# Optimization experiments

Measured on AMD Instinct MI355X. Metric: run time of the kernel, lower is better.

## Reference

```python
import jax, jax.numpy as jnp
import numpy as np

N = 100_000      # num nodes
E = 1_600_000    # num edges
DIN, H, L, NQ = 3, 64, 5, 50_000
BN_EPS = 1e-5


def setup_inputs() -> dict:
    key = jax.random.key(0)
    ks = jax.random.split(key, 24)
    f = lambda k, s, sc=1.0: jax.random.normal(k, s, dtype=jnp.float32) * sc
    inv = 1.0 / np.sqrt(H)
    return {
        "x": f(ks[0], (N, DIN)),
        "edge_index": jax.random.randint(ks[1], (2, E), 0, N, dtype=jnp.int32),
        "n_qubits": NQ,
        "w_in": f(ks[2], (DIN, H), 0.5),
        "b_in": f(ks[3], (H,), 0.1),
        "msg_w1": f(ks[4], (L, H, H), inv),
        "msg_b1": f(ks[5], (L, H), 0.1),
        "msg_w2": f(ks[6], (L, H, H), inv),
        "msg_b2": f(ks[7], (L, H), 0.1),
        "upd_w1": f(ks[8], (L, 2 * H, H), 1.0 / np.sqrt(2 * H)),
        "upd_b1": f(ks[9], (L, H), 0.1),
        "upd_w2": f(ks[10], (L, H, H), inv),
        "upd_b2": f(ks[11], (L, H), 0.1),
        "bn_g": jax.random.uniform(ks[12], (L, H), jnp.float32, 0.5, 1.5),
        "bn_b": f(ks[13], (L, H), 0.1),
        "bn_m": f(ks[14], (L, H), 0.1),
        "bn_v": jax.random.uniform(ks[15], (L, H), jnp.float32, 0.5, 1.5),
        "out_w1": f(ks[16], (H, H // 2), inv),
        "out_b1": f(ks[17], (H // 2,), 0.1),
        "out_w2": f(ks[18], (H // 2, 1), 1.0 / np.sqrt(H // 2)),
        "out_b2": f(ks[19], (1,), 0.1),
    }


def reference(x, edge_index, n_qubits, w_in, b_in,
              msg_w1, msg_b1, msg_w2, msg_b2,
              upd_w1, upd_b1, upd_w2, upd_b2,
              bn_g, bn_b, bn_m, bn_v,
              out_w1, out_b1, out_w2, out_b2):
    src, dst = edge_index[0], edge_index[1]  # PyG: x_j = x[src], aggregate at dst
    h = jax.nn.relu(x @ w_in + b_in)         # [N, H]
    for i in range(L):
        xj = h[src]                                                    # gather [E, H]
        m = jax.nn.relu(xj @ msg_w1[i] + msg_b1[i]) @ msg_w2[i] + msg_b2[i]
        agg = jax.ops.segment_sum(m, dst, num_segments=N)              # scatter-add [N, H]
        comb = jnp.concatenate([h, agg], axis=-1)                      # [N, 2H]
        hn = jax.nn.relu(comb @ upd_w1[i] + upd_b1[i]) @ upd_w2[i] + upd_b2[i]
        # BatchNorm1d (eval mode: running stats) + residual + relu (dropout=eval identity)
        hn = (hn - bn_m[i]) * jax.lax.rsqrt(bn_v[i] + BN_EPS) * bn_g[i] + bn_b[i]
        h = jax.nn.relu(hn + h)
    q = h[:n_qubits]                                                   # qubit nodes [NQ, H]
    return jax.nn.relu(q @ out_w1 + out_b1) @ out_w2 + out_b2          # [NQ, 1]
```

## Files before the change

kernel.cpp:

```cpp
#include <hip/hip_runtime.h>
#include <hip/hip_bf16.h>

#define H 64
#define PADW 88
#define PADT 68
#define CAP 10240
#define WSTRIDE 20480

typedef __attribute__((ext_vector_type(8))) short short8;
typedef __attribute__((ext_vector_type(4))) short short4v;
typedef __attribute__((ext_vector_type(4))) float floatx4;

#define MFMA(a, b, c) __builtin_amdgcn_mfma_f32_16x16x32_bf16(a, b, c, 0, 0, 0)

__device__ __forceinline__ float bf2f(short s) {
  union { unsigned int u; float f; } v;
  v.u = ((unsigned int)(unsigned short)s) << 16;
  return v.f;
}
__device__ __forceinline__ short f2bf(float f) {
  union { float f; unsigned int u; } v; v.f = f;
  unsigned int r = v.u + 0x7fffu + ((v.u >> 16) & 1u);
  return (short)(r >> 16);
}
__device__ __forceinline__ void split2(float v, short& hi, short& lo) {
  hi = f2bf(v);
  lo = f2bf(v - bf2f(hi));
}
__device__ __forceinline__ unsigned int cvtpk(float a, float b) {
  unsigned int r;
  asm("v_cvt_pk_bf16_f32 %0, %1, %2" : "=v"(r) : "v"(a), "v"(b));
  return r;
}
__device__ __forceinline__ short f2bf1(float f) { return (short)cvtpk(f, f); }
__device__ __forceinline__ void split2a(float v, short& hi, short& lo) {
  unsigned int h = cvtpk(v, v);
  union { unsigned int u; float f; } t; t.u = h << 16;
  hi = (short)h;
  float res = v - t.f;
  lo = (short)cvtpk(res, res);
}
__device__ __forceinline__ void split16pk(const float* av, short8* thi, short8* tlo) {
  union U8 { short8 s; unsigned int u[4]; } H0, L0, H1, L1;
#pragma unroll
  for (int p = 0; p < 4; ++p) {
    float v0 = av[2 * p], v1 = av[2 * p + 1];
    unsigned int h = cvtpk(v0, v1);
    union { unsigned int u; float f; } a, b;
    a.u = h << 16; b.u = h & 0xffff0000u;
    H0.u[p] = h; L0.u[p] = cvtpk(v0 - a.f, v1 - b.f);
    float w0 = av[8 + 2 * p], w1 = av[8 + 2 * p + 1];
    unsigned int g = cvtpk(w0, w1);
    union { unsigned int u; float f; } c, d;
    c.u = g << 16; d.u = g & 0xffff0000u;
    H1.u[p] = g; L1.u[p] = cvtpk(w0 - c.f, w1 - d.f);
  }
  thi[0] = H0.s; tlo[0] = L0.s; thi[1] = H1.s; tlo[1] = L1.s;
}
__device__ __forceinline__ float ldf(const void* p, long idx, bool isf32) {
  return isf32 ? ((const float*)p)[idx] : bf2f(((const short*)p)[idx]);
}

__global__ void k_probe(const short* __restrict__ x, int* __restrict__ flag) {
  __shared__ int cnt;
  if (threadIdx.x == 0) cnt = 0;
  __syncthreads();
  short s = x[threadIdx.x];
  int e = (s >> 7) & 0xFF;
  int insane = (e != 0 && (e < 100 || e > 140)) ? 1 : 0;
  atomicAdd(&cnt, insane);
  __syncthreads();
  if (threadIdx.x == 0) *flag = (cnt > 64) ? 1 : 0;
}

__global__ void k_input2(const void* __restrict__ x, const void* __restrict__ w,
                         const void* __restrict__ b, short* __restrict__ hhi,
                         short* __restrict__ hlo, const int* __restrict__ flag, int N) {
  bool isf32 = (*flag != 0);
  int idx = blockIdx.x * 256 + threadIdx.x;
  if (idx >= N * H) return;
  int v = idx >> 6, k = idx & 63;
  float acc = ldf(b, k, isf32);
#pragma unroll
  for (int d = 0; d < 3; ++d)
    acc += ldf(x, (long)v * 3 + d, isf32) * ldf(w, d * 64 + k, isf32);
  float r = fmaxf(acc, 0.f);
  short hi, lo; split2a(r, hi, lo);
  hhi[idx] = hi; hlo[idx] = lo;
}

__global__ void k_prep(const void* __restrict__ U1, const void* __restrict__ U2,
                       const void* __restrict__ W1m, const void* __restrict__ W2m,
                       short* __restrict__ prep, const int* __restrict__ flag) {
  bool isf32 = (*flag != 0);
  int i = blockIdx.x;
  short* p = prep + (long)i * WSTRIDE;
  long oU = (long)i * 8192, oW = (long)i * 4096;
  for (int idx = threadIdx.x; idx < 8192; idx += 256) {
    int in = idx >> 6, n = idx & 63;
    int t = n >> 4, mm = n & 15, c = in >> 5, qq = (in >> 3) & 3, jj = in & 7;
    p[(((t * 4 + c) * 64) + (qq * 16 + mm)) * 8 + jj] = f2bf(ldf(U1, oU + idx, isf32));
  }
  for (int idx = threadIdx.x; idx < 4096; idx += 256) {
    int in = idx >> 6, n = idx & 63;
    int t = n >> 4, mm = n & 15, c = in >> 5, qq = (in >> 3) & 3, jj = in & 7;
    int fi = (((t * 2 + c) * 64) + (qq * 16 + mm)) * 8 + jj;
    p[8192 + fi]  = f2bf(ldf(U2, oW + idx, isf32));
    p[12288 + fi] = f2bf(ldf(W1m, oW + idx, isf32));
    p[16384 + fi] = f2bf(ldf(W2m, oW + idx, isf32));
  }
}


__global__ void k_bcount(const int* __restrict__ dstI, int* __restrict__ bcnt, int E) {
  __shared__ int cl[1024];
  int tid = threadIdx.x;
  for (int t = tid; t < 1024; t += 256) cl[t] = 0;
  __syncthreads();
  for (int i = blockIdx.x * 256 + tid; i < E; i += gridDim.x * 256)
    atomicAdd(&cl[dstI[i] >> 8], 1);
  __syncthreads();
  for (int t = tid; t < 1024; t += 256)
    if (cl[t]) atomicAdd(&bcnt[t], cl[t]);
}

__global__ void k_bscan(const int* __restrict__ bcnt, int* __restrict__ bbase,
                        int* __restrict__ bcur) {
  __shared__ int s[256];
  int tid = threadIdx.x;
  int base = tid * 4;
  int v0 = bcnt[base], v1 = bcnt[base + 1], v2 = bcnt[base + 2], v3 = bcnt[base + 3];
  int tsum = v0 + v1 + v2 + v3;
  s[tid] = tsum;
  __syncthreads();
  for (int off = 1; off < 256; off <<= 1) {
    int x = (tid >= off) ? s[tid - off] : 0;
    __syncthreads();
    s[tid] += x;
    __syncthreads();
  }
  int excl = s[tid] - tsum;
  bbase[base] = excl;           bcur[base] = excl;
  bbase[base + 1] = excl + v0;  bcur[base + 1] = excl + v0;
  bbase[base + 2] = excl + v0 + v1;      bcur[base + 2] = excl + v0 + v1;
  bbase[base + 3] = excl + v0 + v1 + v2; bcur[base + 3] = excl + v0 + v1 + v2;
  if (tid == 255) bbase[1024] = s[255];
}

__global__ void k_bin(const int* __restrict__ srcI, const int* __restrict__ dstI,
                      int* __restrict__ bcur, int2* __restrict__ pairs, int E) {
  __shared__ int cl[1024], cur[1024];
  int tid = threadIdx.x;
  int chunk = (E + gridDim.x - 1) / gridDim.x;
  int s = blockIdx.x * chunk;
  int e = min(s + chunk, E);
  for (int t = tid; t < 1024; t += 256) cl[t] = 0;
  __syncthreads();
  for (int i = s + tid; i < e; i += 256) atomicAdd(&cl[dstI[i] >> 8], 1);
  __syncthreads();
  for (int t = tid; t < 1024; t += 256)
    cur[t] = cl[t] ? atomicAdd(&bcur[t], cl[t]) : 0;
  __syncthreads();
  for (int i = s + tid; i < e; i += 256) {
    int d = dstI[i];
    int p = atomicAdd(&cur[d >> 8], 1);
    pairs[p] = (int2){srcI[i], d};
  }
}

__global__ __launch_bounds__(256) void k_sortb(
    const int2* __restrict__ pairs, const int* __restrict__ bbase,
    int* __restrict__ rowptr, int* __restrict__ srcS, int N, int E, int B) {
  __shared__ int cnt[256], cur[256], s2[256];
  __shared__ int stage[CAP];
  int b = blockIdx.x, tid = threadIdx.x;
  int lo = b << 8;
  int W = min(256, N - lo);
  int s = bbase[b], e = bbase[b + 1];
  cnt[tid] = 0;
  __syncthreads();
  for (int i = s + tid; i < e; i += 256)
    atomicAdd(&cnt[pairs[i].y - lo], 1);
  __syncthreads();
  int v = (tid < W) ? cnt[tid] : 0;
  s2[tid] = v;
  __syncthreads();
  for (int off = 1; off < 256; off <<= 1) {
    int x = (tid >= off) ? s2[tid - off] : 0;
    __syncthreads();
    s2[tid] += x;
    __syncthreads();
  }
  int excl = s2[tid] - v;
  if (tid < W) {
    rowptr[lo + tid] = s + excl;
    cur[tid] = excl;
  }
  if (b == B - 1 && tid == 0) rowptr[N] = E;
  __syncthreads();
  for (int i = s + tid; i < e; i += 256) {
    int2 pr = pairs[i];
    int p = atomicAdd(&cur[pr.y - lo], 1);
    if (p < CAP) stage[p] = pr.x;
    else srcS[s + p] = pr.x;
  }
  __syncthreads();
  int Sb = e - s;
  int lim = Sb < CAP ? Sb : CAP;
  for (int i = tid; i < lim; i += 256) srcS[s + i] = stage[i];
}

__global__ __launch_bounds__(256) void k_mlp(
    const short* __restrict__ hhi, const short* __restrict__ hlo,
    const void* __restrict__ W1, const void* __restrict__ B1,
    const void* __restrict__ W2, long oW, long oB,
    short* __restrict__ M, const int* __restrict__ flag, int N) {
  __shared__ short w1hi[64 * PADW], w1lo[64 * PADW];
  __shared__ short w2hi[64 * PADW], w2lo[64 * PADW];
  __shared__ float b1s[64];
  __shared__ float tbuf[4][16 * PADT];

  bool isf32 = (*flag != 0);
  int tid = threadIdx.x;
  for (int idx = tid; idx < 4096; idx += 256) {
    int j = idx >> 6, k = idx & 63;
    short hi, lo;
    split2a(ldf(W1, oW + idx, isf32), hi, lo);
    w1hi[k * PADW + j] = hi; w1lo[k * PADW + j] = lo;
    split2a(ldf(W2, oW + idx, isf32), hi, lo);
    w2hi[k * PADW + j] = hi; w2lo[k * PADW + j] = lo;
  }
  if (tid < 64) b1s[tid] = ldf(B1, oB + tid, isf32);
  __syncthreads();

  const int wave = tid >> 6, lane = tid & 63;
  const int m = lane & 15, quad = lane >> 4;
  float* tb = tbuf[wave];

  for (int nb = blockIdx.x * 64; nb < N; nb += gridDim.x * 64) {
    const int nBase = nb + wave * 16;
    int node = nBase + m;
    int nc = node < N ? node : N - 1;

    short8 fhi[2], flo[2];
    fhi[0] = *(const short8*)(hhi + (long)nc * H + quad * 8);
    fhi[1] = *(const short8*)(hhi + (long)nc * H + 32 + quad * 8);
    flo[0] = *(const short8*)(hlo + (long)nc * H + quad * 8);
    flo[1] = *(const short8*)(hlo + (long)nc * H + 32 + quad * 8);

    floatx4 acc[4];
#pragma unroll
    for (int t = 0; t < 4; ++t) acc[t] = (floatx4){0.f, 0.f, 0.f, 0.f};
#pragma unroll
    for (int t = 0; t < 4; ++t) {
      const short* whi = &w1hi[(t * 16 + m) * PADW + quad * 8];
      const short* wlo = &w1lo[(t * 16 + m) * PADW + quad * 8];
      acc[t] = MFMA(fhi[0], *(const short8*)(whi), acc[t]);
      acc[t] = MFMA(fhi[1], *(const short8*)(whi + 32), acc[t]);
      acc[t] = MFMA(flo[0], *(const short8*)(whi), acc[t]);
      acc[t] = MFMA(flo[1], *(const short8*)(whi + 32), acc[t]);
      acc[t] = MFMA(fhi[0], *(const short8*)(wlo), acc[t]);
      acc[t] = MFMA(fhi[1], *(const short8*)(wlo + 32), acc[t]);
    }

#pragma unroll
    for (int t = 0; t < 4; ++t) {
      int col = t * 16 + m;
      float bb = b1s[col];
#pragma unroll
      for (int r = 0; r < 4; ++r)
        tb[(quad * 4 + r) * PADT + col] = fmaxf(acc[t][r] + bb, 0.f);
    }

    float av[16];
    *(floatx4*)(av + 0)  = *(const floatx4*)(&tb[m * PADT + quad * 8]);
    *(floatx4*)(av + 4)  = *(const floatx4*)(&tb[m * PADT + quad * 8 + 4]);
    *(floatx4*)(av + 8)  = *(const floatx4*)(&tb[m * PADT + 32 + quad * 8]);
    *(floatx4*)(av + 12) = *(const floatx4*)(&tb[m * PADT + 32 + quad * 8 + 4]);
    short8 thi[2], tlo[2];
    split16pk(av, thi, tlo);

    floatx4 mac[4];
#pragma unroll
    for (int t = 0; t < 4; ++t) mac[t] = (floatx4){0.f, 0.f, 0.f, 0.f};
#pragma unroll
    for (int t = 0; t < 4; ++t) {
      const short* whi = &w2hi[(t * 16 + m) * PADW + quad * 8];
      const short* wlo = &w2lo[(t * 16 + m) * PADW + quad * 8];
      mac[t] = MFMA(thi[0], *(const short8*)(whi), mac[t]);
      mac[t] = MFMA(thi[1], *(const short8*)(whi + 32), mac[t]);
      mac[t] = MFMA(tlo[0], *(const short8*)(whi), mac[t]);
      mac[t] = MFMA(tlo[1], *(const short8*)(whi + 32), mac[t]);
      mac[t] = MFMA(thi[0], *(const short8*)(wlo), mac[t]);
      mac[t] = MFMA(thi[1], *(const short8*)(wlo + 32), mac[t]);
    }

#pragma unroll
    for (int t = 0; t < 4; ++t) {
      int col = t * 16 + m;
#pragma unroll
      for (int r = 0; r < 4; ++r) {
        int nrow = nBase + quad * 4 + r;
        if (nrow < N) M[(long)nrow * H + col] = f2bf1(mac[t][r]);
      }
    }
  }
}

__global__ __launch_bounds__(256) void k_gather(
    const short* __restrict__ M, const int* __restrict__ rowptr,
    const int* __restrict__ srcS, const void* __restrict__ B2, long oB,
    short* __restrict__ agg, const int* __restrict__ flag, int N, int totWaves) {
  __shared__ float b2s[64];
  bool isf32 = (*flag != 0);
  if (threadIdx.x < 64) b2s[threadIdx.x] = ldf(B2, oB + threadIdx.x, isf32);
  __syncthreads();
  const int wave = threadIdx.x >> 6, lane = threadIdx.x & 63;
  const int g = lane >> 3, l = lane & 7;
  float b2v[8];
#pragma unroll
  for (int j = 0; j < 8; ++j) b2v[j] = b2s[l * 8 + j];

  const int gw = blockIdx.x * 4 + wave;
  const int nTask = (N + 7) >> 3;
  for (int task = gw; task < nTask; task += totWaves) {
    int n = task * 8 + g;
    bool valid = n < N;
    int nc = valid ? n : N - 1;
    int rs = rowptr[nc], re = rowptr[nc + 1];
    if (!valid) { rs = 0; re = 0; }
    float a[8];
#pragma unroll
    for (int j = 0; j < 8; ++j) a[j] = 0.f;
    int fullEnd = rs + ((re - rs) & ~7);
    int e = rs;
    for (; e < fullEnd; e += 8) {
      int sv[8];
#pragma unroll
      for (int u = 0; u < 8; ++u) sv[u] = srcS[e + u];
      short8 rr[8];
#pragma unroll
      for (int u = 0; u < 8; ++u)
        rr[u] = *(const short8*)(M + (long)sv[u] * H + l * 8);
#pragma unroll
      for (int u = 0; u < 8; ++u) {
#pragma unroll
        for (int j = 0; j < 8; ++j) a[j] += bf2f(rr[u][j]);
      }
    }
    if (e < re) {
      short8 rr[8];
#pragma unroll
      for (int u = 0; u < 8; ++u) {
        if (e + u < re)
          rr[u] = *(const short8*)(M + (long)srcS[e + u] * H + l * 8);
      }
#pragma unroll
      for (int u = 0; u < 8; ++u) {
        if (e + u < re) {
#pragma unroll
          for (int j = 0; j < 8; ++j) a[j] += bf2f(rr[u][j]);
        }
      }
    }
    if (valid) {
      float dv = (float)(re - rs);
      union { short8 s; unsigned int u[4]; } o;
#pragma unroll
      for (int p = 0; p < 4; ++p)
        o.u[p] = cvtpk(a[2 * p] + dv * b2v[2 * p], a[2 * p + 1] + dv * b2v[2 * p + 1]);
      *(short8*)(agg + (long)n * H + l * 8) = o.s;
    }
  }
}

__global__ __launch_bounds__(512, 4) void k_updm(
    short* __restrict__ hhi, short* __restrict__ hlo, const short* __restrict__ agg,
    const short* __restrict__ pw, const short* __restrict__ pwn,
    const void* __restrict__ UB1, const void* __restrict__ UB2,
    const void* __restrict__ G, const void* __restrict__ Bb,
    const void* __restrict__ Mm, const void* __restrict__ Vv,
    const void* __restrict__ B1m,
    long oB, long oBn,
    short* __restrict__ Mout, const int* __restrict__ flag, int N, int doMsg) {
  __shared__ short u1f[8192];
  __shared__ short u2f[4096];
  __shared__ short m1f[4096];
  __shared__ float b1s[64], b2s[64], scl[64], sft[64], mb1[64];
  __shared__ float tbuf[8][16 * PADT];

  bool isf32 = (*flag != 0);
  int tid = threadIdx.x;
  const int wave = tid >> 6, lane = tid & 63;
  const int m = lane & 15, quad = lane >> 4;

  for (int c = tid; c < 1024; c += 512)
    ((short8*)u1f)[c] = ((const short8*)pw)[c];
  for (int c = tid; c < 512; c += 512) {
    ((short8*)u2f)[c] = ((const short8*)(pw + 8192))[c];
    ((short8*)m1f)[c] = ((const short8*)(pwn + 12288))[c];
  }
  short8 m2r[4][2];
#pragma unroll
  for (int t = 0; t < 4; ++t)
#pragma unroll
    for (int c = 0; c < 2; ++c)
      m2r[t][c] = *(const short8*)&pwn[16384 + (((t * 2 + c) * 64) + lane) * 8];
  if (tid < 64) {
    b1s[tid] = ldf(UB1, oB + tid, isf32);
    b2s[tid] = ldf(UB2, oB + tid, isf32);
    float s = ldf(G, oB + tid, isf32) * rsqrtf(ldf(Vv, oB + tid, isf32) + 1e-5f);
    scl[tid] = s;
    sft[tid] = ldf(Bb, oB + tid, isf32) - ldf(Mm, oB + tid, isf32) * s;
    mb1[tid] = ldf(B1m, oBn + tid, isf32);
  }
  __syncthreads();

  float* tb = tbuf[wave];

  for (int nb = blockIdx.x * 128; nb < N; nb += gridDim.x * 128) {
    const int nBase = nb + wave * 16;
    int node = nBase + m;
    int nc = node < N ? node : N - 1;

    short8 fhi[4], flo[2];
    fhi[0] = *(const short8*)(hhi + (long)nc * H + quad * 8);
    fhi[1] = *(const short8*)(hhi + (long)nc * H + 32 + quad * 8);
    flo[0] = *(const short8*)(hlo + (long)nc * H + quad * 8);
    flo[1] = *(const short8*)(hlo + (long)nc * H + 32 + quad * 8);
    fhi[2] = *(const short8*)(agg + (long)nc * H + quad * 8);
    fhi[3] = *(const short8*)(agg + (long)nc * H + 32 + quad * 8);

    floatx4 acc[4];
#pragma unroll
    for (int t = 0; t < 4; ++t) acc[t] = (floatx4){0.f, 0.f, 0.f, 0.f};
#pragma unroll
    for (int t = 0; t < 4; ++t) {
#pragma unroll
      for (int c = 0; c < 4; ++c) {
        const short8 w = *(const short8*)&u1f[(((t * 4 + c) * 64) + lane) * 8];
        acc[t] = MFMA(fhi[c], w, acc[t]);
        if (c < 2) acc[t] = MFMA(flo[c], w, acc[t]);
      }
    }

#pragma unroll
    for (int t = 0; t < 4; ++t) {
      int col = t * 16 + m;
      float bb = b1s[col];
#pragma unroll
      for (int r = 0; r < 4; ++r)
        tb[(quad * 4 + r) * PADT + col] = fmaxf(acc[t][r] + bb, 0.f);
    }
    float av[16];
    *(floatx4*)(av + 0)  = *(const floatx4*)(&tb[m * PADT + quad * 8]);
    *(floatx4*)(av + 4)  = *(const floatx4*)(&tb[m * PADT + quad * 8 + 4]);
    *(floatx4*)(av + 8)  = *(const floatx4*)(&tb[m * PADT + 32 + quad * 8]);
    *(floatx4*)(av + 12) = *(const floatx4*)(&tb[m * PADT + 32 + quad * 8 + 4]);
    short8 thi[2], tlo[2];
    split16pk(av, thi, tlo);

    floatx4 mac[4];
#pragma unroll
    for (int t = 0; t < 4; ++t) mac[t] = (floatx4){0.f, 0.f, 0.f, 0.f};
#pragma unroll
    for (int t = 0; t < 4; ++t) {
#pragma unroll
      for (int c = 0; c < 2; ++c) {
        const short8 w = *(const short8*)&u2f[(((t * 2 + c) * 64) + lane) * 8];
        mac[t] = MFMA(thi[c], w, mac[t]);
        mac[t] = MFMA(tlo[c], w, mac[t]);
      }
    }

#pragma unroll
    for (int t = 0; t < 4; ++t) {
      int col = t * 16 + m;
      float bb = b2s[col], ss = scl[col], ff = sft[col];
#pragma unroll
      for (int r = 0; r < 4; ++r)
        tb[(quad * 4 + r) * PADT + col] = (mac[t][r] + bb) * ss + ff;
    }
    *(floatx4*)(av + 0)  = *(const floatx4*)(&tb[m * PADT + quad * 8]);
    *(floatx4*)(av + 4)  = *(const floatx4*)(&tb[m * PADT + quad * 8 + 4]);
    *(floatx4*)(av + 8)  = *(const floatx4*)(&tb[m * PADT + 32 + quad * 8]);
    *(floatx4*)(av + 12) = *(const floatx4*)(&tb[m * PADT + 32 + quad * 8 + 4]);
    float hn[16];
#pragma unroll
    for (int j = 0; j < 8; ++j) {
      hn[j]     = fmaxf(av[j]     + bf2f(fhi[0][j]) + bf2f(flo[0][j]), 0.f);
      hn[8 + j] = fmaxf(av[8 + j] + bf2f(fhi[1][j]) + bf2f(flo[1][j]), 0.f);
    }
    split16pk(hn, thi, tlo);
    if (node < N) {
      long base = (long)node * H;
      *(short8*)(hhi + base + quad * 8)      = thi[0];
      *(short8*)(hhi + base + 32 + quad * 8) = thi[1];
      *(short8*)(hlo + base + quad * 8)      = tlo[0];
      *(short8*)(hlo + base + 32 + quad * 8) = tlo[1];
    }

    if (doMsg) {
#pragma unroll
      for (int t = 0; t < 4; ++t) acc[t] = (floatx4){0.f, 0.f, 0.f, 0.f};
#pragma unroll
      for (int t = 0; t < 4; ++t) {
#pragma unroll
        for (int c = 0; c < 2; ++c) {
          const short8 w = *(const short8*)&m1f[(((t * 2 + c) * 64) + lane) * 8];
          acc[t] = MFMA(thi[c], w, acc[t]);
          acc[t] = MFMA(tlo[c], w, acc[t]);
        }
      }

#pragma unroll
      for (int t = 0; t < 4; ++t) {
        int col = t * 16 + m;
        float bb = mb1[col];
#pragma unroll
        for (int r = 0; r < 4; ++r)
          tb[(quad * 4 + r) * PADT + col] = fmaxf(acc[t][r] + bb, 0.f);
      }
      *(floatx4*)(av + 0)  = *(const floatx4*)(&tb[m * PADT + quad * 8]);
      *(floatx4*)(av + 4)  = *(const floatx4*)(&tb[m * PADT + quad * 8 + 4]);
      *(floatx4*)(av + 8)  = *(const floatx4*)(&tb[m * PADT + 32 + quad * 8]);
      *(floatx4*)(av + 12) = *(const floatx4*)(&tb[m * PADT + 32 + quad * 8 + 4]);
      split16pk(av, thi, tlo);

#pragma unroll
      for (int t = 0; t < 4; ++t) mac[t] = (floatx4){0.f, 0.f, 0.f, 0.f};
#pragma unroll
      for (int t = 0; t < 4; ++t) {
#pragma unroll
        for (int c = 0; c < 2; ++c) {
          mac[t] = MFMA(thi[c], m2r[t][c], mac[t]);
          mac[t] = MFMA(tlo[c], m2r[t][c], mac[t]);
        }
      }

#pragma unroll
      for (int t = 0; t < 4; ++t) {
        int col = t * 16 + m;
#pragma unroll
        for (int r = 0; r < 4; ++r)
          tb[(quad * 4 + r) * PADT + col] = mac[t][r];
      }
      *(floatx4*)(av + 0)  = *(const floatx4*)(&tb[m * PADT + quad * 8]);
      *(floatx4*)(av + 4)  = *(const floatx4*)(&tb[m * PADT + quad * 8 + 4]);
      *(floatx4*)(av + 8)  = *(const floatx4*)(&tb[m * PADT + 32 + quad * 8]);
      *(floatx4*)(av + 12) = *(const floatx4*)(&tb[m * PADT + 32 + quad * 8 + 4]);
      if (node < N) {
        union { short8 s; unsigned int u[4]; } M0, M1;
#pragma unroll
        for (int p = 0; p < 4; ++p) {
          M0.u[p] = cvtpk(av[2 * p], av[2 * p + 1]);
          M1.u[p] = cvtpk(av[8 + 2 * p], av[8 + 2 * p + 1]);
        }
        long base = (long)node * H;
        *(short8*)(Mout + base + quad * 8)      = M0.s;
        *(short8*)(Mout + base + 32 + quad * 8) = M1.s;
      }
    }
  }
}

__global__ __launch_bounds__(256) void k_out2(
    const short* __restrict__ hhi, const short* __restrict__ hlo,
    const void* __restrict__ W1, const void* __restrict__ B1,
    const void* __restrict__ W2, const void* __restrict__ B2,
    void* __restrict__ out, const int* __restrict__ flag, int NQ) {
  __shared__ float w1s[64 * 32];
  __shared__ float b1sh[32], w2s[32];
  bool isf32 = (*flag != 0);
  int tid = threadIdx.x;
  for (int idx = tid; idx < 2048; idx += 256) w1s[idx] = ldf(W1, idx, isf32);
  if (tid < 32) { b1sh[tid] = ldf(B1, tid, isf32); w2s[tid] = ldf(W2, tid, isf32); }
  __syncthreads();
  int v = blockIdx.x * 256 + tid;
  if (v >= NQ) return;
  float hr[64];
#pragma unroll
  for (int j = 0; j < 64; ++j)
    hr[j] = bf2f(hhi[(long)v * H + j]) + bf2f(hlo[(long)v * H + j]);
  float accum = ldf(B2, 0, isf32);
#pragma unroll 4
  for (int k = 0; k < 32; ++k) {
    float t = b1sh[k];
#pragma unroll
    for (int j = 0; j < 64; ++j) t += hr[j] * w1s[j * 32 + k];
    accum += fmaxf(t, 0.f) * w2s[k];
  }
  if (isf32) ((float*)out)[v] = accum;
  else ((short*)out)[v] = f2bf1(accum);
}

extern "C" void kernel_launch(void* const* d_in, const int* in_sizes, int n_in,
                              void* d_out, int out_size, void* d_ws, size_t ws_size,
                              hipStream_t stream) {
  const void* x      = d_in[0];
  const int*  ei     = (const int*)d_in[1];
  const void* w_in   = d_in[3];
  const void* b_in   = d_in[4];
  const void* msg_w1 = d_in[5];
  const void* msg_b1 = d_in[6];
  const void* msg_w2 = d_in[7];
  const void* msg_b2 = d_in[8];
  const void* upd_w1 = d_in[9];
  const void* upd_b1 = d_in[10];
  const void* upd_w2 = d_in[11];
  const void* upd_b2 = d_in[12];
  const void* bn_g   = d_in[13];
  const void* bn_b   = d_in[14];
  const void* bn_m   = d_in[15];
  const void* bn_v   = d_in[16];
  const void* out_w1 = d_in[17];
  const void* out_b1 = d_in[18];
  const void* out_w2 = d_in[19];
  const void* out_b2 = d_in[20];

  const int N = in_sizes[0] / 3;
  const int E = in_sizes[1] / 2;
  const int L = in_sizes[5] / (H * H);
  const int* srcI = ei;
  const int* dstI = ei + E;
  const int B = (N + 255) >> 8;

  size_t off = 0;
  auto alloc = [&](size_t bytes) { size_t o = off; off += (bytes + 255) & ~(size_t)255; return o; };
  size_t mSize = (size_t)N * H * sizeof(short);
  size_t pSize = (size_t)E * sizeof(int2);
  size_t o_flag   = alloc(256);
  size_t o_bcnt   = alloc(1024 * sizeof(int));
  size_t o_bbase  = alloc(1025 * sizeof(int));
  size_t o_bcur   = alloc(1024 * sizeof(int));
  size_t o_prep   = alloc((size_t)L * WSTRIDE * sizeof(short));
  size_t o_hhi    = alloc((size_t)N * H * sizeof(short));
  size_t o_hlo    = alloc((size_t)N * H * sizeof(short));
  size_t o_agg    = alloc((size_t)N * H * sizeof(short));
  size_t o_M      = alloc(mSize > pSize ? mSize : pSize);
  size_t o_rowptr = alloc((size_t)(N + 1) * sizeof(int));
  size_t o_srcS   = alloc((size_t)E * sizeof(int));

  char* ws = (char*)d_ws;
  int*   flag   = (int*)(ws + o_flag);
  int*   bcnt   = (int*)(ws + o_bcnt);
  int*   bbase  = (int*)(ws + o_bbase);
  int*   bcur   = (int*)(ws + o_bcur);
  short* prep   = (short*)(ws + o_prep);
  short* hhi    = (short*)(ws + o_hhi);
  short* hlo    = (short*)(ws + o_hlo);
  short* aggS   = (short*)(ws + o_agg);
  short* Mbuf   = (short*)(ws + o_M);
  int2*  pairs  = (int2*)(ws + o_M);
  int*   rowptr = (int*)(ws + o_rowptr);
  int*   srcS   = (int*)(ws + o_srcS);

  k_probe<<<1, 256, 0, stream>>>((const short*)x, flag);
  k_prep<<<L, 256, 0, stream>>>(upd_w1, upd_w2, msg_w1, msg_w2, prep, flag);
  k_input2<<<(N * H + 255) / 256, 256, 0, stream>>>(x, w_in, b_in, hhi, hlo, flag, N);

  hipMemsetAsync(bcnt, 0, 1024 * sizeof(int), stream);
  k_bcount<<<256, 256, 0, stream>>>(dstI, bcnt, E);
  k_bscan<<<1, 256, 0, stream>>>(bcnt, bbase, bcur);
  k_bin<<<256, 256, 0, stream>>>(srcI, dstI, bcur, pairs, E);
  k_sortb<<<B, 256, 0, stream>>>(pairs, bbase, rowptr, srcS, N, E, B);

  k_mlp<<<768, 256, 0, stream>>>(hhi, hlo,
      msg_w1, msg_b1, msg_w2, 0, 0, Mbuf, flag, N);

  const int nTask = (N + 7) >> 3;
  const int GB = (nTask + 7) / 8;
  const int UB = (N + 255) / 256;
  for (int i = 0; i < L; ++i) {
    long oB = (long)i * H;
    int doMsg = (i + 1 < L) ? 1 : 0;
    int iN = doMsg ? i + 1 : i;
    long oBn = doMsg ? (long)(i + 1) * H : 0;
    k_gather<<<GB, 256, 0, stream>>>(Mbuf, rowptr, srcS,
        msg_b2, oB, aggS, flag, N, GB * 4);
    k_updm<<<UB, 512, 0, stream>>>(hhi, hlo, aggS,
        prep + (size_t)i * WSTRIDE, prep + (size_t)iN * WSTRIDE,
        upd_b1, upd_b2, bn_g, bn_b, bn_m, bn_v, msg_b1,
        oB, oBn, Mbuf, flag, N, doMsg);
  }
  k_out2<<<(out_size + 255) / 256, 256, 0, stream>>>(hhi, hlo,
      out_w1, out_b1, out_w2, out_b2, d_out, flag, out_size);
}
```

Measured before the change: 508.8 us.

## Fuse per-layer gather and update kernels into one persistent cooperative kernel

Replaces the per-layer pair of k_gather and k_updm launches with a single cooperative kernel, k_layers, that loops over all layers. Each layer runs a gather phase and an update/message phase, separated by grid-wide barriers. Per-layer weights are reloaded into shared memory inside the loop. This removes repeated kernel launches and the gaps between them, at the cost of grid.sync overhead. It also caps the grid at a size set by occupancy, so the gather phase may run with fewer resident waves than the standalone kernel had.

```diff
diff --git a/kernel.cpp b/kernel.cpp
--- a/kernel.cpp
+++ b/kernel.cpp
@@ -1,5 +1,8 @@
 #include <hip/hip_runtime.h>
 #include <hip/hip_bf16.h>
+#include <hip/hip_cooperative_groups.h>
+
+namespace cg = cooperative_groups;
 
 #define H 64
 #define PADW 88
@@ -22,10 +25,6 @@
   union { float f; unsigned int u; } v; v.f = f;
   unsigned int r = v.u + 0x7fffu + ((v.u >> 16) & 1u);
   return (short)(r >> 16);
-}
-__device__ __forceinline__ void split2(float v, short& hi, short& lo) {
-  hi = f2bf(v);
-  lo = f2bf(v - bf2f(hi));
 }
 __device__ __forceinline__ unsigned int cvtpk(float a, float b) {
   unsigned int r;
@@ -307,82 +306,18 @@
   }
 }
 
-__global__ __launch_bounds__(256) void k_gather(
-    const short* __restrict__ M, const int* __restrict__ rowptr,
-    const int* __restrict__ srcS, const void* __restrict__ B2, long oB,
-    short* __restrict__ agg, const int* __restrict__ flag, int N, int totWaves) {
-  __shared__ float b2s[64];
-  bool isf32 = (*flag != 0);
-  if (threadIdx.x < 64) b2s[threadIdx.x] = ldf(B2, oB + threadIdx.x, isf32);
-  __syncthreads();
-  const int wave = threadIdx.x >> 6, lane = threadIdx.x & 63;
-  const int g = lane >> 3, l = lane & 7;
-  float b2v[8];
-#pragma unroll
-  for (int j = 0; j < 8; ++j) b2v[j] = b2s[l * 8 + j];
-
-  const int gw = blockIdx.x * 4 + wave;
-  const int nTask = (N + 7) >> 3;
-  for (int task = gw; task < nTask; task += totWaves) {
-    int n = task * 8 + g;
-    bool valid = n < N;
-    int nc = valid ? n : N - 1;
-    int rs = rowptr[nc], re = rowptr[nc + 1];
-    if (!valid) { rs = 0; re = 0; }
-    float a[8];
-#pragma unroll
-    for (int j = 0; j < 8; ++j) a[j] = 0.f;
-    int fullEnd = rs + ((re - rs) & ~7);
-    int e = rs;
-    for (; e < fullEnd; e += 8) {
-      int sv[8];
-#pragma unroll
-      for (int u = 0; u < 8; ++u) sv[u] = srcS[e + u];
-      short8 rr[8];
-#pragma unroll
-      for (int u = 0; u < 8; ++u)
-        rr[u] = *(const short8*)(M + (long)sv[u] * H + l * 8);
-#pragma unroll
-      for (int u = 0; u < 8; ++u) {
-#pragma unroll
-        for (int j = 0; j < 8; ++j) a[j] += bf2f(rr[u][j]);
-      }
-    }
-    if (e < re) {
-      short8 rr[8];
-#pragma unroll
-      for (int u = 0; u < 8; ++u) {
-        if (e + u < re)
-          rr[u] = *(const short8*)(M + (long)srcS[e + u] * H + l * 8);
-      }
-#pragma unroll
-      for (int u = 0; u < 8; ++u) {
-        if (e + u < re) {
-#pragma unroll
-          for (int j = 0; j < 8; ++j) a[j] += bf2f(rr[u][j]);
-        }
-      }
-    }
-    if (valid) {
-      float dv = (float)(re - rs);
-      union { short8 s; unsigned int u[4]; } o;
-#pragma unroll
-      for (int p = 0; p < 4; ++p)
-        o.u[p] = cvtpk(a[2 * p] + dv * b2v[2 * p], a[2 * p + 1] + dv * b2v[2 * p + 1]);
-      *(short8*)(agg + (long)n * H + l * 8) = o.s;
-    }
-  }
-}
-
-__global__ __launch_bounds__(512, 4) void k_updm(
-    short* __restrict__ hhi, short* __restrict__ hlo, const short* __restrict__ agg,
-    const short* __restrict__ pw, const short* __restrict__ pwn,
+__global__ __launch_bounds__(512, 4) void k_layers(
+    short* __restrict__ hhi, short* __restrict__ hlo,
+    short* __restrict__ aggS, short* __restrict__ Mbuf,
+    const short* __restrict__ prep, const int* __restrict__ rowptr,
+    const int* __restrict__ srcS,
     const void* __restrict__ UB1, const void* __restrict__ UB2,
     const void* __restrict__ G, const void* __restrict__ Bb,
     const void* __restrict__ Mm, const void* __restrict__ Vv,
-    const void* __restrict__ B1m,
-    long oB, long oBn,
-    short* __restrict__ Mout, const int* __restrict__ flag, int N, int doMsg) {
+    const void* __restrict__ B1m, const void* __restrict__ B2m,
+    const int* __restrict__ flag, int N, int L) {
+  cg::grid_group grid = cg::this_grid();
+
   __shared__ short u1f[8192];
   __shared__ short u2f[4096];
   __shared__ short m1f[4096];
@@ -393,174 +328,244 @@
   int tid = threadIdx.x;
   const int wave = tid >> 6, lane = tid & 63;
   const int m = lane & 15, quad = lane >> 4;
-
-  for (int c = tid; c < 1024; c += 512)
-    ((short8*)u1f)[c] = ((const short8*)pw)[c];
-  for (int c = tid; c < 512; c += 512) {
-    ((short8*)u2f)[c] = ((const short8*)(pw + 8192))[c];
-    ((short8*)m1f)[c] = ((const short8*)(pwn + 12288))[c];
-  }
-  short8 m2r[4][2];
-#pragma unroll
-  for (int t = 0; t < 4; ++t)
-#pragma unroll
-    for (int c = 0; c < 2; ++c)
-      m2r[t][c] = *(const short8*)&pwn[16384 + (((t * 2 + c) * 64) + lane) * 8];
-  if (tid < 64) {
-    b1s[tid] = ldf(UB1, oB + tid, isf32);
-    b2s[tid] = ldf(UB2, oB + tid, isf32);
-    float s = ldf(G, oB + tid, isf32) * rsqrtf(ldf(Vv, oB + tid, isf32) + 1e-5f);
-    scl[tid] = s;
-    sft[tid] = ldf(Bb, oB + tid, isf32) - ldf(Mm, oB + tid, isf32) * s;
-    mb1[tid] = ldf(B1m, oBn + tid, isf32);
-  }
-  __syncthreads();
-
   float* tb = tbuf[wave];
 
-  for (int nb = blockIdx.x * 128; nb < N; nb += gridDim.x * 128) {
-    const int nBase = nb + wave * 16;
-    int node = nBase + m;
-    int nc = node < N ? node : N - 1;
-
-    short8 fhi[4], flo[2];
-    fhi[0] = *(const short8*)(hhi + (long)nc * H + quad * 8);
-    fhi[1] = *(const short8*)(hhi + (long)nc * H + 32 + quad * 8);
-    flo[0] = *(const short8*)(hlo + (long)nc * H + quad * 8);
-    flo[1] = *(const short8*)(hlo + (long)nc * H + 32 + quad * 8);
-    fhi[2] = *(const short8*)(agg + (long)nc * H + quad * 8);
-    fhi[3] = *(const short8*)(agg + (long)nc * H + 32 + quad * 8);
-
-    floatx4 acc[4];
-#pragma unroll
-    for (int t = 0; t < 4; ++t) acc[t] = (floatx4){0.f, 0.f, 0.f, 0.f};
-#pragma unroll
-    for (int t = 0; t < 4; ++t) {
-#pragma unroll
-      for (int c = 0; c < 4; ++c) {
-        const short8 w = *(const short8*)&u1f[(((t * 4 + c) * 64) + lane) * 8];
-        acc[t] = MFMA(fhi[c], w, acc[t]);
-        if (c < 2) acc[t] = MFMA(flo[c], w, acc[t]);
-      }
-    }
-
-#pragma unroll
-    for (int t = 0; t < 4; ++t) {
-      int col = t * 16 + m;
-      float bb = b1s[col];
-#pragma unroll
-      for (int r = 0; r < 4; ++r)
-        tb[(quad * 4 + r) * PADT + col] = fmaxf(acc[t][r] + bb, 0.f);
-    }
-    float av[16];
-    *(floatx4*)(av + 0)  = *(const floatx4*)(&tb[m * PADT + quad * 8]);
-    *(floatx4*)(av + 4)  = *(const floatx4*)(&tb[m * PADT + quad * 8 + 4]);
-    *(floatx4*)(av + 8)  = *(const floatx4*)(&tb[m * PADT + 32 + quad * 8]);
-    *(floatx4*)(av + 12) = *(const floatx4*)(&tb[m * PADT + 32 + quad * 8 + 4]);
-    short8 thi[2], tlo[2];
-    split16pk(av, thi, tlo);
-
-    floatx4 mac[4];
-#pragma unroll
-    for (int t = 0; t < 4; ++t) mac[t] = (floatx4){0.f, 0.f, 0.f, 0.f};
-#pragma unroll
-    for (int t = 0; t < 4; ++t) {
-#pragma unroll
-      for (int c = 0; c < 2; ++c) {
-        const short8 w = *(const short8*)&u2f[(((t * 2 + c) * 64) + lane) * 8];
-        mac[t] = MFMA(thi[c], w, mac[t]);
-        mac[t] = MFMA(tlo[c], w, mac[t]);
-      }
-    }
-
-#pragma unroll
-    for (int t = 0; t < 4; ++t) {
-      int col = t * 16 + m;
-      float bb = b2s[col], ss = scl[col], ff = sft[col];
-#pragma unroll
-      for (int r = 0; r < 4; ++r)
-        tb[(quad * 4 + r) * PADT + col] = (mac[t][r] + bb) * ss + ff;
-    }
-    *(floatx4*)(av + 0)  = *(const floatx4*)(&tb[m * PADT + quad * 8]);
-    *(floatx4*)(av + 4)  = *(const floatx4*)(&tb[m * PADT + quad * 8 + 4]);
-    *(floatx4*)(av + 8)  = *(const floatx4*)(&tb[m * PADT + 32 + quad * 8]);
-    *(floatx4*)(av + 12) = *(const floatx4*)(&tb[m * PADT + 32 + quad * 8 + 4]);
-    float hn[16];
-#pragma unroll
-    for (int j = 0; j < 8; ++j) {
-      hn[j]     = fmaxf(av[j]     + bf2f(fhi[0][j]) + bf2f(flo[0][j]), 0.f);
-      hn[8 + j] = fmaxf(av[8 + j] + bf2f(fhi[1][j]) + bf2f(flo[1][j]), 0.f);
-    }
-    split16pk(hn, thi, tlo);
-    if (node < N) {
-      long base = (long)node * H;
-      *(short8*)(hhi + base + quad * 8)      = thi[0];
-      *(short8*)(hhi + base + 32 + quad * 8) = thi[1];
-      *(short8*)(hlo + base + quad * 8)      = tlo[0];
-      *(short8*)(hlo + base + 32 + quad * 8) = tlo[1];
-    }
-
-    if (doMsg) {
+  for (int i = 0; i < L; ++i) {
+    long oB = (long)i * H;
+    int doMsg = (i + 1 < L) ? 1 : 0;
+    int iN = doMsg ? i + 1 : i;
+    long oBn = doMsg ? (long)(i + 1) * H : 0;
+    const short* pw  = prep + (size_t)i * WSTRIDE;
+    const short* pwn = prep + (size_t)iN * WSTRIDE;
+
+    for (int c = tid; c < 1024; c += 512)
+      ((short8*)u1f)[c] = ((const short8*)pw)[c];
+    for (int c = tid; c < 512; c += 512) {
+      ((short8*)u2f)[c] = ((const short8*)(pw + 8192))[c];
+      ((short8*)m1f)[c] = ((const short8*)(pwn + 12288))[c];
+    }
+    short8 m2r[4][2];
+#pragma unroll
+    for (int t = 0; t < 4; ++t)
+#pragma unroll
+      for (int c = 0; c < 2; ++c)
+        m2r[t][c] = *(const short8*)&pwn[16384 + (((t * 2 + c) * 64) + lane) * 8];
+    if (tid < 64) {
+      b1s[tid] = ldf(UB1, oB + tid, isf32);
+      b2s[tid] = ldf(UB2, oB + tid, isf32);
+      float s = ldf(G, oB + tid, isf32) * rsqrtf(ldf(Vv, oB + tid, isf32) + 1e-5f);
+      scl[tid] = s;
+      sft[tid] = ldf(Bb, oB + tid, isf32) - ldf(Mm, oB + tid, isf32) * s;
+      mb1[tid] = ldf(B1m, oBn + tid, isf32);
+    }
+
+    {
+      const int g = lane >> 3, l = lane & 7;
+      float b2v[8];
+#pragma unroll
+      for (int j = 0; j < 8; ++j) b2v[j] = ldf(B2m, oB + l * 8 + j, isf32);
+      const int totW = gridDim.x * 8;
+      const int gw = blockIdx.x * 8 + wave;
+      const int nTask = (N + 7) >> 3;
+      for (int task = gw; task < nTask; task += totW) {
+        int n = task * 8 + g;
+        bool valid = n < N;
+        int nc2 = valid ? n : N - 1;
+        int rs = rowptr[nc2], re = rowptr[nc2 + 1];
+        if (!valid) { rs = 0; re = 0; }
+        float a[8];
+#pragma unroll
+        for (int j = 0; j < 8; ++j) a[j] = 0.f;
+        int fullEnd = rs + ((re - rs) & ~7);
+        int e = rs;
+        for (; e < fullEnd; e += 8) {
+          int sv[8];
+#pragma unroll
+          for (int u = 0; u < 8; ++u) sv[u] = srcS[e + u];
+          short8 rr[8];
+#pragma unroll
+          for (int u = 0; u < 8; ++u)
+            rr[u] = *(const short8*)(Mbuf + (long)sv[u] * H + l * 8);
+#pragma unroll
+          for (int u = 0; u < 8; ++u) {
+#pragma unroll
+            for (int j = 0; j < 8; ++j) a[j] += bf2f(rr[u][j]);
+          }
+        }
+        if (e < re) {
+          short8 rr[8];
+#pragma unroll
+          for (int u = 0; u < 8; ++u) {
+            if (e + u < re)
+              rr[u] = *(const short8*)(Mbuf + (long)srcS[e + u] * H + l * 8);
+          }
+#pragma unroll
+          for (int u = 0; u < 8; ++u) {
+            if (e + u < re) {
+#pragma unroll
+              for (int j = 0; j < 8; ++j) a[j] += bf2f(rr[u][j]);
+            }
+          }
+        }
+        if (valid) {
+          float dv = (float)(re - rs);
+          union { short8 s; unsigned int u[4]; } o;
+#pragma unroll
+          for (int p = 0; p < 4; ++p)
+            o.u[p] = cvtpk(a[2 * p] + dv * b2v[2 * p], a[2 * p + 1] + dv * b2v[2 * p + 1]);
+          *(short8*)(aggS + (long)n * H + l * 8) = o.s;
+        }
+      }
+    }
+
+    grid.sync();
+
+    for (int nb = blockIdx.x * 128; nb < N; nb += gridDim.x * 128) {
+      const int nBase = nb + wave * 16;
+      int node = nBase + m;
+      int nc = node < N ? node : N - 1;
+
+      short8 fhi[4], flo[2];
+      fhi[0] = *(const short8*)(hhi + (long)nc * H + quad * 8);
+      fhi[1] = *(const short8*)(hhi + (long)nc * H + 32 + quad * 8);
+      flo[0] = *(const short8*)(hlo + (long)nc * H + quad * 8);
+      flo[1] = *(const short8*)(hlo + (long)nc * H + 32 + quad * 8);
+      fhi[2] = *(const short8*)(aggS + (long)nc * H + quad * 8);
+      fhi[3] = *(const short8*)(aggS + (long)nc * H + 32 + quad * 8);
+
+      floatx4 acc[4];
 #pragma unroll
       for (int t = 0; t < 4; ++t) acc[t] = (floatx4){0.f, 0.f, 0.f, 0.f};
 #pragma unroll
       for (int t = 0; t < 4; ++t) {
 #pragma unroll
-        for (int c = 0; c < 2; ++c) {
-          const short8 w = *(const short8*)&m1f[(((t * 2 + c) * 64) + lane) * 8];
-          acc[t] = MFMA(thi[c], w, acc[t]);
-          acc[t] = MFMA(tlo[c], w, acc[t]);
+        for (int c = 0; c < 4; ++c) {
+          const short8 w = *(const short8*)&u1f[(((t * 4 + c) * 64) + lane) * 8];
+          acc[t] = MFMA(fhi[c], w, acc[t]);
+          if (c < 2) acc[t] = MFMA(flo[c], w, acc[t]);
         }
       }
 
 #pragma unroll
       for (int t = 0; t < 4; ++t) {
         int col = t * 16 + m;
-        float bb = mb1[col];
+        float bb = b1s[col];
 #pragma unroll
         for (int r = 0; r < 4; ++r)
           tb[(quad * 4 + r) * PADT + col] = fmaxf(acc[t][r] + bb, 0.f);
       }
+      float av[16];
       *(floatx4*)(av + 0)  = *(const floatx4*)(&tb[m * PADT + quad * 8]);
       *(floatx4*)(av + 4)  = *(const floatx4*)(&tb[m * PADT + quad * 8 + 4]);
       *(floatx4*)(av + 8)  = *(const floatx4*)(&tb[m * PADT + 32 + quad * 8]);
       *(floatx4*)(av + 12) = *(const floatx4*)(&tb[m * PADT + 32 + quad * 8 + 4]);
+      short8 thi[2], tlo[2];
       split16pk(av, thi, tlo);
 
+      floatx4 mac[4];
 #pragma unroll
       for (int t = 0; t < 4; ++t) mac[t] = (floatx4){0.f, 0.f, 0.f, 0.f};
 #pragma unroll
       for (int t = 0; t < 4; ++t) {
 #pragma unroll
         for (int c = 0; c < 2; ++c) {
-          mac[t] = MFMA(thi[c], m2r[t][c], mac[t]);
-          mac[t] = MFMA(tlo[c], m2r[t][c], mac[t]);
+          const short8 w = *(const short8*)&u2f[(((t * 2 + c) * 64) + lane) * 8];
+          mac[t] = MFMA(thi[c], w, mac[t]);
+          mac[t] = MFMA(tlo[c], w, mac[t]);
         }
       }
 
 #pragma unroll
       for (int t = 0; t < 4; ++t) {
         int col = t * 16 + m;
+        float bb = b2s[col], ss = scl[col], ff = sft[col];
 #pragma unroll
         for (int r = 0; r < 4; ++r)
-          tb[(quad * 4 + r) * PADT + col] = mac[t][r];
+          tb[(quad * 4 + r) * PADT + col] = (mac[t][r] + bb) * ss + ff;
       }
       *(floatx4*)(av + 0)  = *(const floatx4*)(&tb[m * PADT + quad * 8]);
       *(floatx4*)(av + 4)  = *(const floatx4*)(&tb[m * PADT + quad * 8 + 4]);
       *(floatx4*)(av + 8)  = *(const floatx4*)(&tb[m * PADT + 32 + quad * 8]);
       *(floatx4*)(av + 12) = *(const floatx4*)(&tb[m * PADT + 32 + quad * 8 + 4]);
+      float hn[16];
+#pragma unroll
+      for (int j = 0; j < 8; ++j) {
+        hn[j]     = fmaxf(av[j]     + bf2f(fhi[0][j]) + bf2f(flo[0][j]), 0.f);
+        hn[8 + j] = fmaxf(av[8 + j] + bf2f(fhi[1][j]) + bf2f(flo[1][j]), 0.f);
+      }
+      split16pk(hn, thi, tlo);
       if (node < N) {
-        union { short8 s; unsigned int u[4]; } M0, M1;
-#pragma unroll
-        for (int p = 0; p < 4; ++p) {
-          M0.u[p] = cvtpk(av[2 * p], av[2 * p + 1]);
-          M1.u[p] = cvtpk(av[8 + 2 * p], av[8 + 2 * p + 1]);
-        }
         long base = (long)node * H;
-        *(short8*)(Mout + base + quad * 8)      = M0.s;
-        *(short8*)(Mout + base + 32 + quad * 8) = M1.s;
-      }
-    }
+        *(short8*)(hhi + base + quad * 8)      = thi[0];
+        *(short8*)(hhi + base + 32 + quad * 8) = thi[1];
+        *(short8*)(hlo + base + quad * 8)      = tlo[0];
+        *(short8*)(hlo + base + 32 + quad * 8) = tlo[1];
+      }
+
+      if (doMsg) {
+#pragma unroll
+        for (int t = 0; t < 4; ++t) acc[t] = (floatx4){0.f, 0.f, 0.f, 0.f};
+#pragma unroll
+        for (int t = 0; t < 4; ++t) {
+#pragma unroll
+          for (int c = 0; c < 2; ++c) {
+            const short8 w = *(const short8*)&m1f[(((t * 2 + c) * 64) + lane) * 8];
+            acc[t] = MFMA(thi[c], w, acc[t]);
+            acc[t] = MFMA(tlo[c], w, acc[t]);
+          }
+        }
+
+#pragma unroll
+        for (int t = 0; t < 4; ++t) {
+          int col = t * 16 + m;
+          float bb = mb1[col];
+#pragma unroll
+          for (int r = 0; r < 4; ++r)
+            tb[(quad * 4 + r) * PADT + col] = fmaxf(acc[t][r] + bb, 0.f);
+        }
+        *(floatx4*)(av + 0)  = *(const floatx4*)(&tb[m * PADT + quad * 8]);
+        *(floatx4*)(av + 4)  = *(const floatx4*)(&tb[m * PADT + quad * 8 + 4]);
+        *(floatx4*)(av + 8)  = *(const floatx4*)(&tb[m * PADT + 32 + quad * 8]);
+        *(floatx4*)(av + 12) = *(const floatx4*)(&tb[m * PADT + 32 + quad * 8 + 4]);
+        split16pk(av, thi, tlo);
+
+#pragma unroll
+        for (int t = 0; t < 4; ++t) mac[t] = (floatx4){0.f, 0.f, 0.f, 0.f};
+#pragma unroll
+        for (int t = 0; t < 4; ++t) {
+#pragma unroll
+          for (int c = 0; c < 2; ++c) {
+            mac[t] = MFMA(thi[c], m2r[t][c], mac[t]);
+            mac[t] = MFMA(tlo[c], m2r[t][c], mac[t]);
+          }
+        }
+
+#pragma unroll
+        for (int t = 0; t < 4; ++t) {
+          int col = t * 16 + m;
+#pragma unroll
+          for (int r = 0; r < 4; ++r)
+            tb[(quad * 4 + r) * PADT + col] = mac[t][r];
+        }
+        *(floatx4*)(av + 0)  = *(const floatx4*)(&tb[m * PADT + quad * 8]);
+        *(floatx4*)(av + 4)  = *(const floatx4*)(&tb[m * PADT + quad * 8 + 4]);
+        *(floatx4*)(av + 8)  = *(const floatx4*)(&tb[m * PADT + 32 + quad * 8]);
+        *(floatx4*)(av + 12) = *(const floatx4*)(&tb[m * PADT + 32 + quad * 8 + 4]);
+        if (node < N) {
+          union { short8 s; unsigned int u[4]; } M0, M1;
+#pragma unroll
+          for (int p = 0; p < 4; ++p) {
+            M0.u[p] = cvtpk(av[2 * p], av[2 * p + 1]);
+            M1.u[p] = cvtpk(av[8 + 2 * p], av[8 + 2 * p + 1]);
+          }
+          long base = (long)node * H;
+          *(short8*)(Mbuf + base + quad * 8)      = M0.s;
+          *(short8*)(Mbuf + base + 32 + quad * 8) = M1.s;
+        }
+      }
+    }
+
+    grid.sync();
   }
 }
 
@@ -620,7 +625,7 @@
 
   const int N = in_sizes[0] / 3;
   const int E = in_sizes[1] / 2;
-  const int L = in_sizes[5] / (H * H);
+  int L = in_sizes[5] / (H * H);
   const int* srcI = ei;
   const int* dstI = ei + E;
   const int B = (N + 255) >> 8;
@@ -668,21 +673,20 @@
   k_mlp<<<768, 256, 0, stream>>>(hhi, hlo,
       msg_w1, msg_b1, msg_w2, 0, 0, Mbuf, flag, N);
 
-  const int nTask = (N + 7) >> 3;
-  const int GB = (nTask + 7) / 8;
-  const int UB = (N + 255) / 256;
-  for (int i = 0; i < L; ++i) {
-    long oB = (long)i * H;
-    int doMsg = (i + 1 < L) ? 1 : 0;
-    int iN = doMsg ? i + 1 : i;
-    long oBn = doMsg ? (long)(i + 1) * H : 0;
-    k_gather<<<GB, 256, 0, stream>>>(Mbuf, rowptr, srcS,
-        msg_b2, oB, aggS, flag, N, GB * 4);
-    k_updm<<<UB, 512, 0, stream>>>(hhi, hlo, aggS,
-        prep + (size_t)i * WSTRIDE, prep + (size_t)iN * WSTRIDE,
-        upd_b1, upd_b2, bn_g, bn_b, bn_m, bn_v, msg_b1,
-        oB, oBn, Mbuf, flag, N, doMsg);
-  }
+  int maxb = 0;
+  hipOccupancyMaxActiveBlocksPerMultiprocessor(&maxb, k_layers, 512, 0);
+  if (maxb < 1) maxb = 1;
+  int UBL = maxb * 256;
+  if (UBL > 512) UBL = 512;
+  void* kargs[] = {
+    (void*)&hhi, (void*)&hlo, (void*)&aggS, (void*)&Mbuf,
+    (void*)&prep, (void*)&rowptr, (void*)&srcS,
+    (void*)&upd_b1, (void*)&upd_b2, (void*)&bn_g, (void*)&bn_b,
+    (void*)&bn_m, (void*)&bn_v, (void*)&msg_b1, (void*)&msg_b2,
+    (void*)&flag, (void*)&N, (void*)&L
+  };
+  hipLaunchCooperativeKernel((void*)k_layers, dim3(UBL), dim3(512), kargs, 0, stream);
+
   k_out2<<<(out_size + 255) / 256, 256, 0, stream>>>(hhi, hlo,
       out_w1, out_b1, out_w2, out_b2, d_out, flag, out_size);
 }
```

Measured after the change: 922.4 us. 81.3% more time.

## Pack edge pairs into one int, vectorize bucket count, use atomic tile scheduler in update

Applied to the files above, without the earlier changes.

Edge (src,dst) pairs are packed into a single 32-bit int (src<<8 | dst low byte), which halves the pair buffer traffic in binning and sorting. The bucket count kernel now reads dst indices as int4. The update kernel switches from a fixed grid over 128-node tiles to a persistent grid of 512 blocks that claim tiles via a global atomic counter, reset in the scan kernel, so weight staging in LDS is amortized over many tiles. The risks are an extra atomic and two barriers per tile, and src<<8 packing only works while node ids stay below 2^23.

```diff
diff --git a/kernel.cpp b/kernel.cpp
--- a/kernel.cpp
+++ b/kernel.cpp
@@ -22,10 +22,6 @@
   union { float f; unsigned int u; } v; v.f = f;
   unsigned int r = v.u + 0x7fffu + ((v.u >> 16) & 1u);
   return (short)(r >> 16);
-}
-__device__ __forceinline__ void split2(float v, short& hi, short& lo) {
-  hi = f2bf(v);
-  lo = f2bf(v - bf2f(hi));
 }
 __device__ __forceinline__ unsigned int cvtpk(float a, float b) {
   unsigned int r;
@@ -117,7 +113,17 @@
   int tid = threadIdx.x;
   for (int t = tid; t < 1024; t += 256) cl[t] = 0;
   __syncthreads();
-  for (int i = blockIdx.x * 256 + tid; i < E; i += gridDim.x * 256)
+  const int stride = gridDim.x * 256;
+  const int nV = E >> 2;
+  const int4* d4 = (const int4*)dstI;
+  for (int i = blockIdx.x * 256 + tid; i < nV; i += stride) {
+    int4 d = d4[i];
+    atomicAdd(&cl[d.x >> 8], 1);
+    atomicAdd(&cl[d.y >> 8], 1);
+    atomicAdd(&cl[d.z >> 8], 1);
+    atomicAdd(&cl[d.w >> 8], 1);
+  }
+  for (int i = (nV << 2) + blockIdx.x * 256 + tid; i < E; i += stride)
     atomicAdd(&cl[dstI[i] >> 8], 1);
   __syncthreads();
   for (int t = tid; t < 1024; t += 256)
@@ -125,9 +131,10 @@
 }
 
 __global__ void k_bscan(const int* __restrict__ bcnt, int* __restrict__ bbase,
-                        int* __restrict__ bcur) {
+                        int* __restrict__ bcur, int* __restrict__ ctr) {
   __shared__ int s[256];
   int tid = threadIdx.x;
+  if (tid < 16) ctr[tid] = 0;
   int base = tid * 4;
   int v0 = bcnt[base], v1 = bcnt[base + 1], v2 = bcnt[base + 2], v3 = bcnt[base + 3];
   int tsum = v0 + v1 + v2 + v3;
@@ -148,7 +155,7 @@
 }
 
 __global__ void k_bin(const int* __restrict__ srcI, const int* __restrict__ dstI,
-                      int* __restrict__ bcur, int2* __restrict__ pairs, int E) {
+                      int* __restrict__ bcur, int* __restrict__ pairs, int E) {
   __shared__ int cl[1024], cur[1024];
   int tid = threadIdx.x;
   int chunk = (E + gridDim.x - 1) / gridDim.x;
@@ -164,12 +171,12 @@
   for (int i = s + tid; i < e; i += 256) {
     int d = dstI[i];
     int p = atomicAdd(&cur[d >> 8], 1);
-    pairs[p] = (int2){srcI[i], d};
+    pairs[p] = (srcI[i] << 8) | (d & 255);
   }
 }
 
 __global__ __launch_bounds__(256) void k_sortb(
-    const int2* __restrict__ pairs, const int* __restrict__ bbase,
+    const int* __restrict__ pairs, const int* __restrict__ bbase,
     int* __restrict__ rowptr, int* __restrict__ srcS, int N, int E, int B) {
   __shared__ int cnt[256], cur[256], s2[256];
   __shared__ int stage[CAP];
@@ -180,7 +187,7 @@
   cnt[tid] = 0;
   __syncthreads();
   for (int i = s + tid; i < e; i += 256)
-    atomicAdd(&cnt[pairs[i].y - lo], 1);
+    atomicAdd(&cnt[pairs[i] & 255], 1);
   __syncthreads();
   int v = (tid < W) ? cnt[tid] : 0;
   s2[tid] = v;
@@ -199,10 +206,10 @@
   if (b == B - 1 && tid == 0) rowptr[N] = E;
   __syncthreads();
   for (int i = s + tid; i < e; i += 256) {
-    int2 pr = pairs[i];
-    int p = atomicAdd(&cur[pr.y - lo], 1);
-    if (p < CAP) stage[p] = pr.x;
-    else srcS[s + p] = pr.x;
+    int pr = pairs[i];
+    int p = atomicAdd(&cur[pr & 255], 1);
+    if (p < CAP) stage[p] = pr >> 8;
+    else srcS[s + p] = pr >> 8;
   }
   __syncthreads();
   int Sb = e - s;
@@ -382,12 +389,14 @@
     const void* __restrict__ Mm, const void* __restrict__ Vv,
     const void* __restrict__ B1m,
     long oB, long oBn,
-    short* __restrict__ Mout, const int* __restrict__ flag, int N, int doMsg) {
+    short* __restrict__ Mout, int* __restrict__ ctr,
+    const int* __restrict__ flag, int N, int doMsg) {
   __shared__ short u1f[8192];
   __shared__ short u2f[4096];
   __shared__ short m1f[4096];
   __shared__ float b1s[64], b2s[64], scl[64], sft[64], mb1[64];
   __shared__ float tbuf[8][16 * PADT];
+  __shared__ int s_t;
 
   bool isf32 = (*flag != 0);
   int tid = threadIdx.x;
@@ -414,11 +423,10 @@
     sft[tid] = ldf(Bb, oB + tid, isf32) - ldf(Mm, oB + tid, isf32) * s;
     mb1[tid] = ldf(B1m, oBn + tid, isf32);
   }
-  __syncthreads();
 
   float* tb = tbuf[wave];
 
-  for (int nb = blockIdx.x * 128; nb < N; nb += gridDim.x * 128) {
+  auto processT = [&](int nb) {
     const int nBase = nb + wave * 16;
     int node = nBase + m;
     int nc = node < N ? node : N - 1;
@@ -561,6 +569,16 @@
         *(short8*)(Mout + base + 32 + quad * 8) = M1.s;
       }
     }
+  };
+
+  const int nTiles = (N + 127) >> 7;
+  for (;;) {
+    __syncthreads();
+    if (tid == 0) s_t = atomicAdd(ctr, 1);
+    __syncthreads();
+    int t = s_t;
+    if (t >= nTiles) break;
+    processT(t << 7);
   }
 }
 
@@ -628,11 +646,12 @@
   size_t off = 0;
   auto alloc = [&](size_t bytes) { size_t o = off; off += (bytes + 255) & ~(size_t)255; return o; };
   size_t mSize = (size_t)N * H * sizeof(short);
-  size_t pSize = (size_t)E * sizeof(int2);
+  size_t pSize = (size_t)E * sizeof(int);
   size_t o_flag   = alloc(256);
   size_t o_bcnt   = alloc(1024 * sizeof(int));
   size_t o_bbase  = alloc(1025 * sizeof(int));
   size_t o_bcur   = alloc(1024 * sizeof(int));
+  size_t o_ctr    = alloc(16 * sizeof(int));
   size_t o_prep   = alloc((size_t)L * WSTRIDE * sizeof(short));
   size_t o_hhi    = alloc((size_t)N * H * sizeof(short));
   size_t o_hlo    = alloc((size_t)N * H * sizeof(short));
@@ -646,12 +665,13 @@
   int*   bcnt   = (int*)(ws + o_bcnt);
   int*   bbase  = (int*)(ws + o_bbase);
   int*   bcur   = (int*)(ws + o_bcur);
+  int*   ctr    = (int*)(ws + o_ctr);
   short* prep   = (short*)(ws + o_prep);
   short* hhi    = (short*)(ws + o_hhi);
   short* hlo    = (short*)(ws + o_hlo);
   short* aggS   = (short*)(ws + o_agg);
   short* Mbuf   = (short*)(ws + o_M);
-  int2*  pairs  = (int2*)(ws + o_M);
+  int*   pairs  = (int*)(ws + o_M);
   int*   rowptr = (int*)(ws + o_rowptr);
   int*   srcS   = (int*)(ws + o_srcS);
 
@@ -661,7 +681,7 @@
 
   hipMemsetAsync(bcnt, 0, 1024 * sizeof(int), stream);
   k_bcount<<<256, 256, 0, stream>>>(dstI, bcnt, E);
-  k_bscan<<<1, 256, 0, stream>>>(bcnt, bbase, bcur);
+  k_bscan<<<1, 256, 0, stream>>>(bcnt, bbase, bcur, ctr);
   k_bin<<<256, 256, 0, stream>>>(srcI, dstI, bcur, pairs, E);
   k_sortb<<<B, 256, 0, stream>>>(pairs, bbase, rowptr, srcS, N, E, B);
 
@@ -670,7 +690,7 @@
 
   const int nTask = (N + 7) >> 3;
   const int GB = (nTask + 7) / 8;
-  const int UB = (N + 255) / 256;
+  const int UB = 512;
   for (int i = 0; i < L; ++i) {
     long oB = (long)i * H;
     int doMsg = (i + 1 < L) ? 1 : 0;
@@ -681,7 +701,7 @@
     k_updm<<<UB, 512, 0, stream>>>(hhi, hlo, aggS,
         prep + (size_t)i * WSTRIDE, prep + (size_t)iN * WSTRIDE,
         upd_b1, upd_b2, bn_g, bn_b, bn_m, bn_v, msg_b1,
-        oB, oBn, Mbuf, flag, N, doMsg);
+        oB, oBn, Mbuf, ctr + i, flag, N, doMsg);
   }
   k_out2<<<(out_size + 255) / 256, 256, 0, stream>>>(hhi, hlo,
       out_w1, out_b1, out_w2, out_b2, d_out, flag, out_size);
```

New measurement: 537.9 us. 5.7% more time.
